# Optimization experiments

Measured on AMD Instinct MI355X. Metric: run time of the kernel, lower is better.

## Reference

```python
import jax, jax.numpy as jnp
import numpy as np

D_MODEL = 512
N_HEADS = 8
D_K = D_MODEL // N_HEADS
LN_EPS = 1e-5


def setup_inputs() -> dict:
    key = jax.random.key(0)
    ks = jax.random.split(key, 8)
    B, S, D = 2, 4096, D_MODEL
    # xavier_uniform bound for square [D, D] weight
    bound = float(np.sqrt(6.0 / (D + D)))
    x = jax.random.normal(ks[0], (B, S, D), dtype=jnp.float32)
    w_q = jax.random.uniform(ks[1], (D, D), jnp.float32, -bound, bound)
    w_k = jax.random.uniform(ks[2], (D, D), jnp.float32, -bound, bound)
    w_v = jax.random.uniform(ks[3], (D, D), jnp.float32, -bound, bound)
    # w_o: torch Linear default init (kaiming-uniform-ish); uniform is fine as data
    lim = float(1.0 / np.sqrt(D))
    w_o = jax.random.uniform(ks[4], (D, D), jnp.float32, -lim, lim)
    b_o = jax.random.uniform(ks[5], (D,), jnp.float32, -lim, lim)
    ln_gamma = jnp.ones((D,), jnp.float32)
    ln_beta = jnp.zeros((D,), jnp.float32)
    return {"x": x, "w_q": w_q, "w_k": w_k, "w_v": w_v,
            "w_o": w_o, "b_o": b_o, "ln_gamma": ln_gamma, "ln_beta": ln_beta}


def _layer_norm(x, gamma, beta):
    mu = jnp.mean(x, axis=-1, keepdims=True)
    var = jnp.mean(jnp.square(x - mu), axis=-1, keepdims=True)
    return (x - mu) * jax.lax.rsqrt(var + LN_EPS) * gamma + beta


def reference(x, w_q, w_k, w_v, w_o, b_o, ln_gamma, ln_beta):
    B, S, D = x.shape
    residual = x
    h = _layer_norm(x, ln_gamma, ln_beta)
    # torch Linear: y = h @ W.T ; reshape to [B, H, S, d_k]
    def proj(W):
        return (h @ W.T).reshape(B, S, N_HEADS, D_K).transpose(0, 2, 1, 3)
    Q, K, V = proj(w_q), proj(w_k), proj(w_v)
    scores = jnp.einsum('bhqd,bhkd->bhqk', Q, K) / jnp.sqrt(jnp.float32(D_K))
    attn = jax.nn.softmax(scores, axis=-1)  # dropout p=0 -> identity
    attended = jnp.einsum('bhqk,bhkd->bhqd', attn, V)
    attended = attended.transpose(0, 2, 1, 3).reshape(B, S, D)
    out = attended @ w_o.T + b_o
    return out + residual
```

## Files before the change

### kernel.cpp

```cpp
#include <hip/hip_runtime.h>
#include <hip/hip_bf16.h>
#include <stdint.h>


typedef __bf16 bf16;
typedef __attribute__((ext_vector_type(8))) __bf16 bf16x8;
typedef __attribute__((ext_vector_type(4))) __bf16 bf16x4;
typedef __attribute__((ext_vector_type(4))) float f32x4;
typedef __attribute__((ext_vector_type(4))) short s16x4;

#define LOG2E 1.44269504088896340736f
#define SW(row, grp) (((row) << 6) + ((((grp) ^ ((row) & 7))) << 3))

__device__ __forceinline__ f32x4 pv_mfma16(bf16x4 v, bf16x4 p, f32x4 c) {
#if __has_builtin(__builtin_amdgcn_mfma_f32_16x16x16bf16_1k)
  return __builtin_amdgcn_mfma_f32_16x16x16bf16_1k(
      __builtin_bit_cast(s16x4, v), __builtin_bit_cast(s16x4, p), c, 0, 0, 0);
#elif __has_builtin(__builtin_amdgcn_mfma_f32_16x16x16_bf16)
  return __builtin_amdgcn_mfma_f32_16x16x16_bf16(v, p, c, 0, 0, 0);
#else
  f32x4 d;
  asm("v_mfma_f32_16x16x16_bf16 %0, %1, %2, %3"
      : "=v"(d) : "v"(v), "v"(p), "v"(c));
  return d;
#endif
}

__global__ __launch_bounds__(256) void ln_kernel(
    const float* __restrict__ x, const float* __restrict__ gamma,
    const float* __restrict__ beta, bf16* __restrict__ h) {
  int wave = threadIdx.x >> 6, lane = threadIdx.x & 63;
  int row = blockIdx.x * 4 + wave;
  const float* xr = x + (size_t)row * 512 + lane * 8;
  f32x4 v0 = *(const f32x4*)xr;
  f32x4 v1 = *(const f32x4*)(xr + 4);
  float f[8], s = 0.f, s2 = 0.f;
#pragma unroll
  for (int i = 0; i < 4; ++i) { f[i] = v0[i]; f[4 + i] = v1[i]; }
#pragma unroll
  for (int i = 0; i < 8; ++i) { s += f[i]; s2 += f[i] * f[i]; }
#pragma unroll
  for (int off = 1; off < 64; off <<= 1) {
    s  += __shfl_xor(s, off, 64);
    s2 += __shfl_xor(s2, off, 64);
  }
  float mu  = s * (1.f / 512.f);
  float var = s2 * (1.f / 512.f) - mu * mu;
  float rstd = rsqrtf(var + 1e-5f);
  f32x4 g0 = *(const f32x4*)(gamma + lane * 8);
  f32x4 g1 = *(const f32x4*)(gamma + lane * 8 + 4);
  f32x4 b0 = *(const f32x4*)(beta + lane * 8);
  f32x4 b1 = *(const f32x4*)(beta + lane * 8 + 4);
  bf16x8 o;
#pragma unroll
  for (int i = 0; i < 4; ++i) {
    o[i]     = (bf16)((f[i]     - mu) * rstd * g0[i] + b0[i]);
    o[4 + i] = (bf16)((f[4 + i] - mu) * rstd * g1[i] + b1[i]);
  }
  *(bf16x8*)(h + (size_t)row * 512 + lane * 8) = o;
}

__global__ __launch_bounds__(256) void qkv_kernel(
    const bf16* __restrict__ h, const float* __restrict__ wq,
    const float* __restrict__ wk, const float* __restrict__ wv,
    bf16* __restrict__ Qg, bf16* __restrict__ Kg, bf16* __restrict__ Vtg) {
  __shared__ bf16 As[128 * 64];
  __shared__ bf16 Bs[128 * 64];
  int tid = threadIdx.x, wave = tid >> 6, lane = tid & 63;
  int wm = wave >> 1, wn = wave & 1, quad = lane >> 4, l15 = lane & 15;
  int mtile = blockIdx.x;
  int wsel = blockIdx.y >> 2;
  int nb = blockIdx.y & 3;
  const float* W = (wsel == 0) ? wq : (wsel == 1 ? wk : wv);
  const bf16*  Abase = h + (size_t)mtile * 128 * 512;
  const float* Bbase = W + (size_t)nb * 128 * 512;
  f32x4 acc[4][4];
#pragma unroll
  for (int i = 0; i < 4; ++i)
#pragma unroll
    for (int j = 0; j < 4; ++j) acc[i][j] = (f32x4){0.f, 0.f, 0.f, 0.f};

  int srow = tid >> 3, grp = tid & 7, scol = grp * 8;
  bf16x8 ar[4];
  f32x4 br0[4], br1[4];
#pragma unroll
  for (int k = 0; k < 4; ++k) {
    int rr = srow + k * 32;
    ar[k]  = *(const bf16x8*)(Abase + (size_t)rr * 512 + scol);
    br0[k] = *(const f32x4*)(Bbase + (size_t)rr * 512 + scol);
    br1[k] = *(const f32x4*)(Bbase + (size_t)rr * 512 + scol + 4);
  }
  for (int k0 = 0; k0 < 512; k0 += 64) {
#pragma unroll
    for (int k = 0; k < 4; ++k) {
      int rr = srow + k * 32;
      int w = SW(rr, grp);
      *(bf16x8*)(As + w) = ar[k];
      bf16x8 wb;
#pragma unroll
      for (int j = 0; j < 4; ++j) { wb[j] = (bf16)br0[k][j]; wb[4 + j] = (bf16)br1[k][j]; }
      *(bf16x8*)(Bs + w) = wb;
    }
    __syncthreads();
    if (k0 < 448) {
#pragma unroll
      for (int k = 0; k < 4; ++k) {
        int rr = srow + k * 32;
        ar[k]  = *(const bf16x8*)(Abase + (size_t)rr * 512 + k0 + 64 + scol);
        br0[k] = *(const f32x4*)(Bbase + (size_t)rr * 512 + k0 + 64 + scol);
        br1[k] = *(const f32x4*)(Bbase + (size_t)rr * 512 + k0 + 64 + scol + 4);
      }
    }
#pragma unroll
    for (int c = 0; c < 2; ++c) {
      bf16x8 af[4], bw[4];
#pragma unroll
      for (int mt = 0; mt < 4; ++mt)
        af[mt] = *(const bf16x8*)(As + SW(wm * 64 + mt * 16 + l15, c * 4 + quad));
#pragma unroll
      for (int nt = 0; nt < 4; ++nt)
        bw[nt] = *(const bf16x8*)(Bs + SW(wn * 64 + nt * 16 + l15, c * 4 + quad));
#pragma unroll
      for (int mt = 0; mt < 4; ++mt)
#pragma unroll
        for (int nt = 0; nt < 4; ++nt)
          acc[mt][nt] = __builtin_amdgcn_mfma_f32_16x16x32_bf16(
              bw[nt], af[mt], acc[mt][nt], 0, 0, 0);
    }
    __syncthreads();
  }
  float qscale = (wsel == 0) ? (0.125f * LOG2E) : 1.0f;
#pragma unroll
  for (int mt = 0; mt < 4; ++mt) {
    int m_g = mtile * 128 + wm * 64 + mt * 16 + l15;
    int b = m_g >> 12, s = m_g & 4095;
#pragma unroll
    for (int nt = 0; nt < 4; ++nt) {
      int n_g = nb * 128 + wn * 64 + nt * 16 + quad * 4;
      int head = n_g >> 6, d = n_g & 63;
      f32x4 a = acc[mt][nt];
      if (wsel < 2) {
        bf16* dst = (wsel == 0 ? Qg : Kg) +
                    ((size_t)((b * 8 + head) * 4096 + s)) * 64 + d;
        bf16x4 pk;
#pragma unroll
        for (int r = 0; r < 4; ++r) pk[r] = (bf16)(a[r] * qscale);
        *(bf16x4*)dst = pk;
      } else {
        bf16* dst = Vtg + ((size_t)((b * 8 + head) * 64 + d)) * 4096 + s;
#pragma unroll
        for (int r = 0; r < 4; ++r) dst[(size_t)r * 4096] = (bf16)a[r];
      }
    }
  }
}

__global__ __launch_bounds__(256, 2) void attn_kernel(
    const bf16* __restrict__ Qg, const bf16* __restrict__ Kg,
    const bf16* __restrict__ Vtg, bf16* __restrict__ Og) {
  __shared__ char smem[64 * 1024];
  bf16* KV = (bf16*)smem;
  float* OL = (float*)smem;
  float* Ll = (float*)(smem + 49152);

  int tid = threadIdx.x, wave = tid >> 6, lane = tid & 63;
  int quad = lane >> 4, l15 = lane & 15;
  int qgrp = wave & 1, khalf = wave >> 1;
  int q0 = blockIdx.x * 128;
  int bh = blockIdx.y;
  int hi = bh & 7, bi = bh >> 3;
  const bf16* Kh  = Kg  + (size_t)bh * 4096 * 64;
  const bf16* Vth = Vtg + (size_t)bh * 64 * 4096;

  bf16x8 qf[4][2];
#pragma unroll
  for (int mt = 0; mt < 4; ++mt)
#pragma unroll
    for (int c = 0; c < 2; ++c)
      qf[mt][c] = *(const bf16x8*)(
          Qg + ((size_t)bh * 4096 + q0 + qgrp * 64 + mt * 16 + l15) * 64 +
          c * 32 + quad * 8);

  f32x4 o_acc[4][4];
  float l_part[4] = {0.f, 0.f, 0.f, 0.f};
#pragma unroll
  for (int mt = 0; mt < 4; ++mt)
#pragma unroll
    for (int nt = 0; nt < 4; ++nt) o_acc[mt][nt] = (f32x4){0.f, 0.f, 0.f, 0.f};

  bf16* sbase = KV + khalf * 8192 + (qgrp ? 4096 : 0);
  bf16x8 sr[8];
  int key0 = khalf * 2048;
#pragma unroll
  for (int i = 0; i < 8; ++i) {
    int e = i * 512 + lane * 8;
    sr[i] = qgrp
        ? *(const bf16x8*)(Vth + (size_t)(e >> 6) * 4096 + key0 + (e & 63))
        : *(const bf16x8*)(Kh + (size_t)key0 * 64 + e);
  }
#pragma unroll
  for (int i = 0; i < 8; ++i) {
    int e = i * 512 + lane * 8;
    *(bf16x8*)(sbase + SW(e >> 6, (e >> 3) & 7)) = sr[i];
  }
#pragma unroll
  for (int i = 0; i < 8; ++i) {
    int e = i * 512 + lane * 8;
    sr[i] = qgrp
        ? *(const bf16x8*)(Vth + (size_t)(e >> 6) * 4096 + key0 + 64 + (e & 63))
        : *(const bf16x8*)(Kh + (size_t)(key0 + 64) * 64 + e);
  }
  __syncthreads();

  for (int kt = 0; kt < 32; ++kt) {
    int cur = kt & 1, nxt = cur ^ 1;
    bf16* Ksw = KV + cur * 16384 + khalf * 8192;
    bf16* Vsw = Ksw + 4096;
    if (kt < 31) {
#pragma unroll
      for (int i = 0; i < 8; ++i) {
        int e = i * 512 + lane * 8;
        *(bf16x8*)(sbase + nxt * 16384 + SW(e >> 6, (e >> 3) & 7)) = sr[i];
      }
    }
    if (kt < 30) {
      int kbase = key0 + (kt + 2) * 64;
#pragma unroll
      for (int i = 0; i < 8; ++i) {
        int e = i * 512 + lane * 8;
        sr[i] = qgrp
            ? *(const bf16x8*)(Vth + (size_t)(e >> 6) * 4096 + kbase + (e & 63))
            : *(const bf16x8*)(Kh + (size_t)kbase * 64 + e);
      }
    }
    bf16x8 kf[8];
#pragma unroll
    for (int kb = 0; kb < 4; ++kb)
#pragma unroll
      for (int c = 0; c < 2; ++c)
        kf[kb * 2 + c] = *(const bf16x8*)(Ksw + SW(kb * 16 + l15, c * 4 + quad));
    bf16x4 vf[16];
#pragma unroll
    for (int kb = 0; kb < 4; ++kb)
#pragma unroll
      for (int nt = 0; nt < 4; ++nt)
        vf[kb * 4 + nt] = *(const bf16x4*)(
            &Vsw[SW(nt * 16 + l15, kb * 2 + (quad >> 1)) + (quad & 1) * 4]);
#pragma unroll
    for (int mt = 0; mt < 4; ++mt) {
      f32x4 st[4];
#pragma unroll
      for (int kb = 0; kb < 4; ++kb) st[kb] = (f32x4){0.f, 0.f, 0.f, 0.f};
#pragma unroll
      for (int c = 0; c < 2; ++c)
#pragma unroll
        for (int kb = 0; kb < 4; ++kb)
          st[kb] = __builtin_amdgcn_mfma_f32_16x16x32_bf16(
              kf[kb * 2 + c], qf[mt][c], st[kb], 0, 0, 0);
#pragma unroll
      for (int kb = 0; kb < 4; ++kb) {
        bf16x4 pk;
#pragma unroll
        for (int r = 0; r < 4; ++r) {
          float pv = __builtin_amdgcn_exp2f(st[kb][r]);
          l_part[mt] += pv;
          pk[r] = (bf16)pv;
        }
#pragma unroll
        for (int nt = 0; nt < 4; ++nt)
          o_acc[mt][nt] = pv_mfma16(vf[kb * 4 + nt], pk, o_acc[mt][nt]);
      }
    }
    __syncthreads();
  }
#pragma unroll
  for (int mt = 0; mt < 4; ++mt) {
    l_part[mt] += __shfl_xor(l_part[mt], 16, 64);
    l_part[mt] += __shfl_xor(l_part[mt], 32, 64);
  }
  if (khalf == 1) {
    float* dst = OL + qgrp * 4096;
#pragma unroll
    for (int mt = 0; mt < 4; ++mt) {
#pragma unroll
      for (int nt = 0; nt < 4; ++nt) {
        int row = mt * 16 + l15;
        int g = nt * 4 + quad;
        int gs = (g & 8) | ((g ^ row) & 7);
        *(f32x4*)(&dst[row * 64 + gs * 4]) = o_acc[mt][nt];
      }
      if (quad == 0) Ll[qgrp * 64 + mt * 16 + l15] = l_part[mt];
    }
  }
  __syncthreads();
  if (khalf == 0) {
    const float* src = OL + qgrp * 4096;
#pragma unroll
    for (int mt = 0; mt < 4; ++mt) {
      float lt = l_part[mt] + Ll[qgrp * 64 + mt * 16 + l15];
      float inv = 1.0f / lt;
      int q = q0 + qgrp * 64 + mt * 16 + l15;
#pragma unroll
      for (int nt = 0; nt < 4; ++nt) {
        int row = mt * 16 + l15;
        int g = nt * 4 + quad;
        int gs = (g & 8) | ((g ^ row) & 7);
        f32x4 o = *(const f32x4*)(&src[row * 64 + gs * 4]);
        bf16x4 pk;
#pragma unroll
        for (int r = 0; r < 4; ++r)
          pk[r] = (bf16)((o[r] + o_acc[mt][nt][r]) * inv);
        *(bf16x4*)(&Og[((size_t)bi * 4096 + q) * 512 + hi * 64 + nt * 16 +
                       quad * 4]) = pk;
      }
    }
  }
}

__global__ __launch_bounds__(256) void proj_kernel(
    const bf16* __restrict__ A, const float* __restrict__ Wo,
    const float* __restrict__ bo, const float* __restrict__ x,
    float* __restrict__ out) {
  __shared__ bf16 As[128 * 64];
  __shared__ bf16 Bs[128 * 64];
  int tid = threadIdx.x, wave = tid >> 6, lane = tid & 63;
  int wm = wave >> 1, wn = wave & 1, quad = lane >> 4, l15 = lane & 15;
  int mtile = blockIdx.x, nb = blockIdx.y;
  const bf16*  Abase = A + (size_t)mtile * 128 * 512;
  const float* Bbase = Wo + (size_t)nb * 128 * 512;
  f32x4 acc[4][4];
#pragma unroll
  for (int i = 0; i < 4; ++i)
#pragma unroll
    for (int j = 0; j < 4; ++j) acc[i][j] = (f32x4){0.f, 0.f, 0.f, 0.f};

  int srow = tid >> 3, grp = tid & 7, scol = grp * 8;
  bf16x8 ar[4];
  f32x4 br0[4], br1[4];
#pragma unroll
  for (int k = 0; k < 4; ++k) {
    int rr = srow + k * 32;
    ar[k]  = *(const bf16x8*)(Abase + (size_t)rr * 512 + scol);
    br0[k] = *(const f32x4*)(Bbase + (size_t)rr * 512 + scol);
    br1[k] = *(const f32x4*)(Bbase + (size_t)rr * 512 + scol + 4);
  }
  for (int k0 = 0; k0 < 512; k0 += 64) {
#pragma unroll
    for (int k = 0; k < 4; ++k) {
      int rr = srow + k * 32;
      int w = SW(rr, grp);
      *(bf16x8*)(As + w) = ar[k];
      bf16x8 wb;
#pragma unroll
      for (int j = 0; j < 4; ++j) { wb[j] = (bf16)br0[k][j]; wb[4 + j] = (bf16)br1[k][j]; }
      *(bf16x8*)(Bs + w) = wb;
    }
    __syncthreads();
    if (k0 < 448) {
#pragma unroll
      for (int k = 0; k < 4; ++k) {
        int rr = srow + k * 32;
        ar[k]  = *(const bf16x8*)(Abase + (size_t)rr * 512 + k0 + 64 + scol);
        br0[k] = *(const f32x4*)(Bbase + (size_t)rr * 512 + k0 + 64 + scol);
        br1[k] = *(const f32x4*)(Bbase + (size_t)rr * 512 + k0 + 64 + scol + 4);
      }
    }
#pragma unroll
    for (int c = 0; c < 2; ++c) {
      bf16x8 af[4], bw[4];
#pragma unroll
      for (int mt = 0; mt < 4; ++mt)
        af[mt] = *(const bf16x8*)(As + SW(wm * 64 + mt * 16 + l15, c * 4 + quad));
#pragma unroll
      for (int nt = 0; nt < 4; ++nt)
        bw[nt] = *(const bf16x8*)(Bs + SW(wn * 64 + nt * 16 + l15, c * 4 + quad));
#pragma unroll
      for (int mt = 0; mt < 4; ++mt)
#pragma unroll
        for (int nt = 0; nt < 4; ++nt)
          acc[mt][nt] = __builtin_amdgcn_mfma_f32_16x16x32_bf16(
              bw[nt], af[mt], acc[mt][nt], 0, 0, 0);
    }
    __syncthreads();
  }
#pragma unroll
  for (int mt = 0; mt < 4; ++mt) {
    int m_g = mtile * 128 + wm * 64 + mt * 16 + l15;
#pragma unroll
    for (int nt = 0; nt < 4; ++nt) {
      int n_g = nb * 128 + wn * 64 + nt * 16 + quad * 4;
      f32x4 a = acc[mt][nt];
      f32x4 xr = *(const f32x4*)(x + (size_t)m_g * 512 + n_g);
      f32x4 bb = *(const f32x4*)(bo + n_g);
      f32x4 o;
#pragma unroll
      for (int r = 0; r < 4; ++r)
        o[r] = a[r] + bb[r] + xr[r];
      *(f32x4*)(out + (size_t)m_g * 512 + n_g) = o;
    }
  }
}

extern "C" void kernel_launch(void* const* d_in, const int* in_sizes, int n_in,
                              void* d_out, int out_size, void* d_ws, size_t ws_size,
                              hipStream_t stream) {
  const float* x     = (const float*)d_in[0];
  const float* wq    = (const float*)d_in[1];
  const float* wk    = (const float*)d_in[2];
  const float* wv    = (const float*)d_in[3];
  const float* wo    = (const float*)d_in[4];
  const float* bo    = (const float*)d_in[5];
  const float* gamma = (const float*)d_in[6];
  const float* beta  = (const float*)d_in[7];
  float* out = (float*)d_out;
  char* ws = (char*)d_ws;
  const size_t SZ = (size_t)8192 * 512 * sizeof(bf16);
  bf16* h   = (bf16*)(ws);
  bf16* Ao  = (bf16*)(ws);
  bf16* Qg  = (bf16*)(ws + SZ);
  bf16* Kg  = (bf16*)(ws + 2 * SZ);
  bf16* Vtg = (bf16*)(ws + 3 * SZ);

  ln_kernel<<<2048, 256, 0, stream>>>(x, gamma, beta, h);
  qkv_kernel<<<dim3(64, 12), 256, 0, stream>>>(h, wq, wk, wv, Qg, Kg, Vtg);
  attn_kernel<<<dim3(32, 16), 256, 0, stream>>>(Qg, Kg, Vtg, Ao);
  proj_kernel<<<dim3(64, 4), 256, 0, stream>>>(Ao, wo, bo, x, out);
}
```

Baseline: 210.0 us.

## Use 16x16x32 MFMA for PV, compute row sums via MFMA, remap grid

Replaces the 16x16x16 PV MFMAs with 16x16x32 MFMAs by pairing two key blocks into 8-wide bf16 fragments. The softmax row sums are now produced by an extra MFMA against a ones vector, which removes the per-element scalar adds and the cross-lane shuffle reduction. Float-to-bf16 packing uses a byte permute, so it truncates instead of rounding. The grid is flattened and remapped so neighbouring blocks take different heads and batches, changing the order in which K/V are reused from cache; the trade-off is slightly lower precision and extra MFMA work for the sums.

New measurement: 191.0 us. -9.1%, faster.

```diff
diff --git a/kernel.cpp b/kernel.cpp
--- a/kernel.cpp
+++ b/kernel.cpp
@@ -7,23 +7,15 @@
 typedef __attribute__((ext_vector_type(8))) __bf16 bf16x8;
 typedef __attribute__((ext_vector_type(4))) __bf16 bf16x4;
 typedef __attribute__((ext_vector_type(4))) float f32x4;
-typedef __attribute__((ext_vector_type(4))) short s16x4;
+typedef __attribute__((ext_vector_type(4))) unsigned int u32x4;
 
 #define LOG2E 1.44269504088896340736f
 #define SW(row, grp) (((row) << 6) + ((((grp) ^ ((row) & 7))) << 3))
 
-__device__ __forceinline__ f32x4 pv_mfma16(bf16x4 v, bf16x4 p, f32x4 c) {
-#if __has_builtin(__builtin_amdgcn_mfma_f32_16x16x16bf16_1k)
-  return __builtin_amdgcn_mfma_f32_16x16x16bf16_1k(
-      __builtin_bit_cast(s16x4, v), __builtin_bit_cast(s16x4, p), c, 0, 0, 0);
-#elif __has_builtin(__builtin_amdgcn_mfma_f32_16x16x16_bf16)
-  return __builtin_amdgcn_mfma_f32_16x16x16_bf16(v, p, c, 0, 0, 0);
-#else
-  f32x4 d;
-  asm("v_mfma_f32_16x16x16_bf16 %0, %1, %2, %3"
-      : "=v"(d) : "v"(v), "v"(p), "v"(c));
-  return d;
-#endif
+__device__ __forceinline__ unsigned int pkbf16(float lo, float hi) {
+  return __builtin_amdgcn_perm(__builtin_bit_cast(unsigned int, hi),
+                               __builtin_bit_cast(unsigned int, lo),
+                               0x07060302u);
 }
 
 __global__ __launch_bounds__(256) void ln_kernel(
@@ -166,8 +158,9 @@
   int tid = threadIdx.x, wave = tid >> 6, lane = tid & 63;
   int quad = lane >> 4, l15 = lane & 15;
   int qgrp = wave & 1, khalf = wave >> 1;
-  int q0 = blockIdx.x * 128;
-  int bh = blockIdx.y;
+  int lin = blockIdx.x;
+  int bh = ((lin & 7) << 1) | ((lin >> 3) & 1);
+  int q0 = (lin >> 4) * 128;
   int hi = bh & 7, bi = bh >> 3;
   const bf16* Kh  = Kg  + (size_t)bh * 4096 * 64;
   const bf16* Vth = Vtg + (size_t)bh * 64 * 4096;
@@ -181,12 +174,15 @@
           Qg + ((size_t)bh * 4096 + q0 + qgrp * 64 + mt * 16 + l15) * 64 +
           c * 32 + quad * 8);
 
-  f32x4 o_acc[4][4];
-  float l_part[4] = {0.f, 0.f, 0.f, 0.f};
-#pragma unroll
-  for (int mt = 0; mt < 4; ++mt)
+  f32x4 o_acc[4][4], lacc[4];
+#pragma unroll
+  for (int mt = 0; mt < 4; ++mt) {
+    lacc[mt] = (f32x4){0.f, 0.f, 0.f, 0.f};
 #pragma unroll
     for (int nt = 0; nt < 4; ++nt) o_acc[mt][nt] = (f32x4){0.f, 0.f, 0.f, 0.f};
+  }
+  const u32x4 onesu = {0x3F803F80u, 0x3F803F80u, 0x3F803F80u, 0x3F803F80u};
+  const bf16x8 ones8 = __builtin_bit_cast(bf16x8, onesu);
 
   bf16* sbase = KV + khalf * 8192 + (qgrp ? 4096 : 0);
   bf16x8 sr[8];
@@ -239,13 +235,20 @@
 #pragma unroll
       for (int c = 0; c < 2; ++c)
         kf[kb * 2 + c] = *(const bf16x8*)(Ksw + SW(kb * 16 + l15, c * 4 + quad));
-    bf16x4 vf[16];
-#pragma unroll
-    for (int kb = 0; kb < 4; ++kb)
-#pragma unroll
-      for (int nt = 0; nt < 4; ++nt)
-        vf[kb * 4 + nt] = *(const bf16x4*)(
-            &Vsw[SW(nt * 16 + l15, kb * 2 + (quad >> 1)) + (quad & 1) * 4]);
+    bf16x8 vf8[2][4];
+#pragma unroll
+    for (int pr = 0; pr < 2; ++pr)
+#pragma unroll
+      for (int nt = 0; nt < 4; ++nt) {
+        bf16x4 lo = *(const bf16x4*)(
+            &Vsw[SW(nt * 16 + l15, (pr * 2) * 2 + (quad >> 1)) + (quad & 1) * 4]);
+        bf16x4 hi4 = *(const bf16x4*)(
+            &Vsw[SW(nt * 16 + l15, (pr * 2 + 1) * 2 + (quad >> 1)) + (quad & 1) * 4]);
+        bf16x8 v;
+#pragma unroll
+        for (int j = 0; j < 4; ++j) { v[j] = lo[j]; v[4 + j] = hi4[j]; }
+        vf8[pr][nt] = v;
+      }
 #pragma unroll
     for (int mt = 0; mt < 4; ++mt) {
       f32x4 st[4];
@@ -258,25 +261,25 @@
           st[kb] = __builtin_amdgcn_mfma_f32_16x16x32_bf16(
               kf[kb * 2 + c], qf[mt][c], st[kb], 0, 0, 0);
 #pragma unroll
-      for (int kb = 0; kb < 4; ++kb) {
-        bf16x4 pk;
+      for (int pr = 0; pr < 2; ++pr) {
+        float ea[4], eb[4];
 #pragma unroll
         for (int r = 0; r < 4; ++r) {
-          float pv = __builtin_amdgcn_exp2f(st[kb][r]);
-          l_part[mt] += pv;
-          pk[r] = (bf16)pv;
+          ea[r] = __builtin_amdgcn_exp2f(st[pr * 2][r]);
+          eb[r] = __builtin_amdgcn_exp2f(st[pr * 2 + 1][r]);
         }
+        u32x4 pw = {pkbf16(ea[0], ea[1]), pkbf16(ea[2], ea[3]),
+                    pkbf16(eb[0], eb[1]), pkbf16(eb[2], eb[3])};
+        bf16x8 pk8 = __builtin_bit_cast(bf16x8, pw);
 #pragma unroll
         for (int nt = 0; nt < 4; ++nt)
-          o_acc[mt][nt] = pv_mfma16(vf[kb * 4 + nt], pk, o_acc[mt][nt]);
+          o_acc[mt][nt] = __builtin_amdgcn_mfma_f32_16x16x32_bf16(
+              vf8[pr][nt], pk8, o_acc[mt][nt], 0, 0, 0);
+        lacc[mt] = __builtin_amdgcn_mfma_f32_16x16x32_bf16(
+            ones8, pk8, lacc[mt], 0, 0, 0);
       }
     }
     __syncthreads();
-  }
-#pragma unroll
-  for (int mt = 0; mt < 4; ++mt) {
-    l_part[mt] += __shfl_xor(l_part[mt], 16, 64);
-    l_part[mt] += __shfl_xor(l_part[mt], 32, 64);
   }
   if (khalf == 1) {
     float* dst = OL + qgrp * 4096;
@@ -289,7 +292,7 @@
         int gs = (g & 8) | ((g ^ row) & 7);
         *(f32x4*)(&dst[row * 64 + gs * 4]) = o_acc[mt][nt];
       }
-      if (quad == 0) Ll[qgrp * 64 + mt * 16 + l15] = l_part[mt];
+      if (quad == 0) Ll[qgrp * 64 + mt * 16 + l15] = lacc[mt][0];
     }
   }
   __syncthreads();
@@ -297,7 +300,7 @@
     const float* src = OL + qgrp * 4096;
 #pragma unroll
     for (int mt = 0; mt < 4; ++mt) {
-      float lt = l_part[mt] + Ll[qgrp * 64 + mt * 16 + l15];
+      float lt = lacc[mt][0] + Ll[qgrp * 64 + mt * 16 + l15];
       float inv = 1.0f / lt;
       int q = q0 + qgrp * 64 + mt * 16 + l15;
 #pragma unroll
@@ -423,6 +426,6 @@
 
   ln_kernel<<<2048, 256, 0, stream>>>(x, gamma, beta, h);
   qkv_kernel<<<dim3(64, 12), 256, 0, stream>>>(h, wq, wk, wv, Qg, Kg, Vtg);
-  attn_kernel<<<dim3(32, 16), 256, 0, stream>>>(Qg, Kg, Vtg, Ao);
+  attn_kernel<<<512, 256, 0, stream>>>(Qg, Kg, Vtg, Ao);
   proj_kernel<<<dim3(64, 4), 256, 0, stream>>>(Ao, wo, bo, x, out);
 }
```
